# Kernel tuning notes

Hardware: AMD Instinct MI355X
Metric: run time of the kernel (lower is better)

Reference implementation:

```python
import jax, jax.numpy as jnp
import numpy as np

B, T, D_IN, H, K, C = 8, 2048, 512, 384, 8192, 8
N_BLOCKS = 6
EPS = 1e-5


def conv1d(x, w, b, pad, groups=1):
    # x: [B, Cin, T], w: [Cout, Cin//groups, k]
    y = jax.lax.conv_general_dilated(
        x, w, window_strides=(1,), padding=[(pad, pad)],
        dimension_numbers=("NCH", "OIH", "NCH"), feature_group_count=groups)
    return y + b[None, :, None]


def layernorm(x, g, b):
    # normalize over last axis
    m = jnp.mean(x, axis=-1, keepdims=True)
    v = jnp.mean(jnp.square(x - m), axis=-1, keepdims=True)
    return (x - m) * jax.lax.rsqrt(v + EPS) * g + b


def setup_inputs() -> dict:
    key = jax.random.key(0)
    ks = iter(jax.random.split(key, 32))
    s = 0.02
    inp = {
        "x": jax.random.normal(next(ks), (B, T, D_IN), dtype=jnp.float32),
        "enc_w": jax.random.normal(next(ks), (H, D_IN, 7)) * s,
        "enc_b": jnp.zeros((H,)),
        "enc_ln_g": jnp.ones((H,)),
        "enc_ln_b": jnp.zeros((H,)),
        "blk_dw_w": jax.random.normal(next(ks), (N_BLOCKS, H, 1, 7)) * s,
        "blk_dw_b": jnp.zeros((N_BLOCKS, H)),
        "blk_ln_g": jnp.ones((N_BLOCKS, H)),
        "blk_ln_b": jnp.zeros((N_BLOCKS, H)),
        "blk_w1": jax.random.normal(next(ks), (N_BLOCKS, 4 * H, H)) * s,
        "blk_b1": jnp.zeros((N_BLOCKS, 4 * H)),
        "blk_w2": jax.random.normal(next(ks), (N_BLOCKS, H, 4 * H)) * s,
        "blk_b2": jnp.zeros((N_BLOCKS, H)),
        "out_w": jax.random.normal(next(ks), (C, H, 1)) * s,
        "out_b": jnp.zeros((C,)),
        "embeddings": jax.random.normal(next(ks), (K, C)),
    }
    return inp


def encode(x, enc_w, enc_b, enc_ln_g, enc_ln_b, blk_dw_w, blk_dw_b,
           blk_ln_g, blk_ln_b, blk_w1, blk_b1, blk_w2, blk_b2, out_w, out_b):
    h = x.transpose(0, 2, 1)                       # [B, D_IN, T]
    h = conv1d(h, enc_w, enc_b, pad=3)             # [B, H, T]
    h = layernorm(h.transpose(0, 2, 1), enc_ln_g, enc_ln_b).transpose(0, 2, 1)
    for i in range(N_BLOCKS):
        res = h
        h = conv1d(h, blk_dw_w[i], blk_dw_b[i], pad=3, groups=H)  # depthwise
        ht = h.transpose(0, 2, 1)                  # [B, T, H]
        ht = layernorm(ht, blk_ln_g[i], blk_ln_b[i])
        ht = jnp.einsum("bth,fh->btf", ht, blk_w1[i]) + blk_b1[i]
        ht = jax.nn.gelu(ht, approximate=False)    # torch GELU is exact erf
        ht = jnp.einsum("btf,hf->bth", ht, blk_w2[i]) + blk_b2[i]
        h = ht.transpose(0, 2, 1) + res
    z = conv1d(h, out_w, out_b, pad=0)             # [B, C, T]
    return z.transpose(0, 2, 1)                    # [B, T, C]


def reference(x, enc_w, enc_b, enc_ln_g, enc_ln_b, blk_dw_w, blk_dw_b,
              blk_ln_g, blk_ln_b, blk_w1, blk_b1, blk_w2, blk_b2,
              out_w, out_b, embeddings):
    z = encode(x, enc_w, enc_b, enc_ln_g, enc_ln_b, blk_dw_w, blk_dw_b,
               blk_ln_g, blk_ln_b, blk_w1, blk_b1, blk_w2, blk_b2, out_w, out_b)
    flat = z.reshape(-1, C)                        # [B*T, C]
    # squared euclidean distances: same argmin as torch.cdist
    d2 = (jnp.sum(flat * flat, axis=1, keepdims=True)
          - 2.0 * flat @ embeddings.T
          + jnp.sum(embeddings * embeddings, axis=1))  # [B*T, K]
    indices = jnp.argmin(d2, axis=1)               # [B*T], int
    return indices
```

## Files before the change

kernel.cpp:

```cpp
#include <hip/hip_runtime.h>
#include <math.h>

#define T_   2048
#define DIN  512
#define H_   384
#define H4_  1536
#define BT_  16384

typedef _Float16 half_t;
typedef _Float16 f16x8 __attribute__((ext_vector_type(8)));
typedef _Float16 f16x4 __attribute__((ext_vector_type(4)));
typedef float f32x4 __attribute__((ext_vector_type(4)));

#define LO_SCALE 2048.0f
#define LO_INV   4.8828125e-4f

__device__ __forceinline__ void lds_barrier() {
    asm volatile("s_waitcnt lgkmcnt(0)\n\ts_barrier" ::: "memory");
}

__device__ __forceinline__ void gload_lds(const half_t* g, half_t* l) {
    __builtin_amdgcn_global_load_lds(
        (const __attribute__((address_space(1))) unsigned int*)(const void*)g,
        (__attribute__((address_space(3))) unsigned int*)(void*)l, 16, 0, 0);
}

__device__ __forceinline__ void split2(float v, half_t* hi, half_t* lo) {
    half_t h = (half_t)v;
    *hi = h;
    *lo = (half_t)((v - (float)h) * LO_SCALE);
}

__global__ void k_split4(const float* __restrict__ in, half_t* __restrict__ hi,
                         half_t* __restrict__ lo, long n4) {
    long i = (long)blockIdx.x * 256 + threadIdx.x;
    if (i >= n4) return;
    float4 v = ((const float4*)in)[i];
    f16x4 vh, vl;
    float a[4] = {v.x, v.y, v.z, v.w};
#pragma unroll
    for (int j = 0; j < 4; ++j) {
        half_t h = (half_t)a[j];
        vh[j] = h;
        vl[j] = (half_t)((a[j] - (float)h) * LO_SCALE);
    }
    ((f16x4*)hi)[i] = vh;
    ((f16x4*)lo)[i] = vl;
}

__global__ void k_split_encw(const float* __restrict__ in, half_t* __restrict__ hi,
                             half_t* __restrict__ lo) {
    int idx = blockIdx.x * 256 + threadIdx.x;
    if (idx >= H_ * 3584) return;
    int n = idx / 3584;
    int r = idx % 3584;
    int tap = r >> 9, i = r & 511;
    split2(in[n * 3584 + i * 7 + tap], hi + idx, lo + idx);
}

__global__ void k_ln(const float* __restrict__ in, float* __restrict__ out,
                     const float* __restrict__ g, const float* __restrict__ b) {
    int row = blockIdx.x;
    int lane = threadIdx.x;
    const float* ir = in + (long)row * H_;
    float v[6];
    float s = 0.f;
#pragma unroll
    for (int j = 0; j < 6; ++j) { v[j] = ir[lane + (j << 6)]; s += v[j]; }
#pragma unroll
    for (int o = 32; o > 0; o >>= 1) s += __shfl_down(s, o, 64);
    s = __shfl(s, 0, 64);
    float mean = s * (1.f / 384.f);
    float q = 0.f;
#pragma unroll
    for (int j = 0; j < 6; ++j) { float d = v[j] - mean; q += d * d; }
#pragma unroll
    for (int o = 32; o > 0; o >>= 1) q += __shfl_down(q, o, 64);
    q = __shfl(q, 0, 64);
    float rstd = rsqrtf(q * (1.f / 384.f) + 1e-5f);
    float* orow = out + (long)row * H_;
#pragma unroll
    for (int j = 0; j < 6; ++j) {
        int c = lane + (j << 6);
        orow[c] = (v[j] - mean) * rstd * g[c] + b[c];
    }
}

__global__ __launch_bounds__(256) void k_dwconv_ln(
    const float* __restrict__ h, half_t* __restrict__ oh,
    half_t* __restrict__ ol,
    const float* __restrict__ w, const float* __restrict__ wb,
    const float* __restrict__ g, const float* __restrict__ gb) {
    int row = (blockIdx.x << 2) + (threadIdx.x >> 6);
    int b = row >> 11;
    int t = row & 2047;
    int lane = threadIdx.x & 63;
    const float* hb = h + ((long)b * T_) * H_;
    float vx[3], vy[3];
    float s = 0.f;
#pragma unroll
    for (int j = 0; j < 3; ++j) {
        int c = (lane << 1) + (j << 7);
        float ax = wb[c], ay = wb[c + 1];
        const float* wcx = w + c * 7;
        const float* wcy = wcx + 7;
#pragma unroll
        for (int k = 0; k < 7; ++k) {
            int tt = t + k - 3;
            if ((unsigned)tt < (unsigned)T_) {
                float2 hv = *(const float2*)&hb[(long)tt * H_ + c];
                ax = fmaf(hv.x, wcx[k], ax);
                ay = fmaf(hv.y, wcy[k], ay);
            }
        }
        vx[j] = ax; vy[j] = ay;
        s += ax + ay;
    }
#pragma unroll
    for (int o = 32; o > 0; o >>= 1) s += __shfl_down(s, o, 64);
    s = __shfl(s, 0, 64);
    float mean = s * (1.f / 384.f);
    float q = 0.f;
#pragma unroll
    for (int j = 0; j < 3; ++j) {
        float dx = vx[j] - mean, dy = vy[j] - mean;
        q += dx * dx + dy * dy;
    }
#pragma unroll
    for (int o = 32; o > 0; o >>= 1) q += __shfl_down(q, o, 64);
    q = __shfl(q, 0, 64);
    float rstd = rsqrtf(q * (1.f / 384.f) + 1e-5f);
    long ro = (long)row * H_;
#pragma unroll
    for (int j = 0; j < 3; ++j) {
        int c = (lane << 1) + (j << 7);
        float valx = (vx[j] - mean) * rstd * g[c] + gb[c];
        float valy = (vy[j] - mean) * rstd * g[c + 1] + gb[c + 1];
        split2(valx, oh + ro + c, ol + ro + c);
        split2(valy, oh + ro + c + 1, ol + ro + c + 1);
    }
}

#define DECLSET(S) float4 pAh##S, pAl##S, pBh0##S, pBl0##S, pBh1##S, pBl1##S

#define LOADREGS(S, k0_) do {                                               \
    int k0v = (k0_);                                                        \
    if (MODE == 0) {                                                        \
        int kk = k0v + ak;                                                  \
        int tap = kk >> 9, ii = kk & 511;                                   \
        int ta = tt0 + tap;                                                 \
        pAh##S = pAl##S = make_float4(0.f, 0.f, 0.f, 0.f);                  \
        if ((unsigned)ta < 2048u) {                                         \
            long o = ((long)bq * 2048 + ta) * 512 + ii;                     \
            pAh##S = *(const float4*)(Ah + o);                              \
            pAl##S = *(const float4*)(Al + o);                              \
        }                                                                   \
    } else {                                                                \
        pAh##S = *(const float4*)(Ah + aoff + k0v);                         \
        pAl##S = *(const float4*)(Al + aoff + k0v);                         \
    }                                                                       \
    pBh0##S = *(const float4*)(Bh + boff0 + k0v);                           \
    pBl0##S = *(const float4*)(Bl + boff0 + k0v);                           \
    pBh1##S = *(const float4*)(Bh + boff1 + k0v);                           \
    pBl1##S = *(const float4*)(Bl + boff1 + k0v);                           \
} while (0)

#define STOREBUF(S, buf) do {                                               \
    *(float4*)&smem[(buf) * 2048 + aw] = pAh##S;                            \
    *(float4*)&smem[4096 + (buf) * 2048 + aw] = pAl##S;                     \
    int b_ = 8192 + (buf) * 4096 + aw;                                      \
    *(float4*)&smem[b_] = pBh0##S;                                          \
    *(float4*)&smem[b_ + 2048] = pBh1##S;                                   \
    *(float4*)&smem[b_ + 8192] = pBl0##S;                                   \
    *(float4*)&smem[b_ + 8192 + 2048] = pBl1##S;                            \
} while (0)

template <int MODE, int NN>
__global__ __launch_bounds__(256, 3) void k_mgemm64(
    const half_t* __restrict__ Ah, const half_t* __restrict__ Al,
    const half_t* __restrict__ Bh, const half_t* __restrict__ Bl,
    const float* __restrict__ bias, const float* __restrict__ res,
    float* __restrict__ Cf, half_t* __restrict__ Ch, half_t* __restrict__ Cl,
    int N, int K) {
    __shared__ __align__(16) half_t smem[24576];
    const int tid = threadIdx.x;
    const int lane = tid & 63, wid = tid >> 6;
    const int wn = wid << 5;
    const int quad = lane >> 4, l16 = lane & 15;

    constexpr int NWG = 256 * NN;
    constexpr int CHUNK = NWG / 8;
    const int lin = blockIdx.x;
    const int tile = (lin & 7) * CHUNK + (lin >> 3);
    const int m0 = (tile / NN) << 6;
    const int n0 = (tile % NN) << 7;

    const int ar = tid >> 2;
    const int ak = (tid & 3) << 3;

    long aoff = 0;
    int tt0 = 0, bq = 0;
    if (MODE == 0) {
        bq = m0 >> 11;
        tt0 = (m0 & 2047) + ar - 3;
    } else {
        aoff = (long)(m0 + ar) * K + ak;
    }
    const long boff0 = (long)(n0 + ar) * K + ak;
    const long boff1 = boff0 + (long)64 * K;

    const int aw = ar * 32 + ((((tid & 3) ^ (ar >> 1)) & 3) << 3);

    DECLSET(0);
    DECLSET(1);

    f32x4 acc1[4][2] = {};
    f32x4 acc2[4][2] = {};
    const int sw = ((quad ^ (l16 >> 1)) & 3) << 3;

    auto compute = [&](int buf) {
        const int ab = buf * 2048 + l16 * 32 + sw;
        const int bb = 8192 + buf * 4096 + (wn + l16) * 32 + sw;
        f16x8 fah[4], fal[4], fgh[2], fgl[2];
#pragma unroll
        for (int f = 0; f < 4; ++f) {
            fah[f] = *(const f16x8*)&smem[ab + f * 512];
            fal[f] = *(const f16x8*)&smem[ab + 4096 + f * 512];
        }
#pragma unroll
        for (int g = 0; g < 2; ++g) {
            fgh[g] = *(const f16x8*)&smem[bb + g * 512];
            fgl[g] = *(const f16x8*)&smem[bb + 8192 + g * 512];
        }
#pragma unroll
        for (int f = 0; f < 4; ++f)
#pragma unroll
            for (int g = 0; g < 2; ++g)
                acc2[f][g] = __builtin_amdgcn_mfma_f32_16x16x32_f16(fah[f], fgl[g], acc2[f][g], 0, 0, 0);
#pragma unroll
        for (int f = 0; f < 4; ++f)
#pragma unroll
            for (int g = 0; g < 2; ++g)
                acc2[f][g] = __builtin_amdgcn_mfma_f32_16x16x32_f16(fal[f], fgh[g], acc2[f][g], 0, 0, 0);
#pragma unroll
        for (int f = 0; f < 4; ++f)
#pragma unroll
            for (int g = 0; g < 2; ++g)
                acc1[f][g] = __builtin_amdgcn_mfma_f32_16x16x32_f16(fah[f], fgh[g], acc1[f][g], 0, 0, 0);
    };

    const int nIter = K >> 5;
    LOADREGS(0, 0);
    LOADREGS(1, 32);
    STOREBUF(0, 0);
    if (nIter > 2) LOADREGS(0, 64);
    for (int it = 0; it < nIter; it += 2) {
        lds_barrier();
        compute(0);
        STOREBUF(1, 1);
        if (it + 3 < nIter) LOADREGS(1, (it + 3) << 5);
        lds_barrier();
        compute(1);
        if (it + 2 < nIter) {
            STOREBUF(0, 0);
            if (it + 4 < nIter) LOADREGS(0, (it + 4) << 5);
        }
    }

    float bv[2];
    bv[0] = bias[n0 + wn + l16];
    bv[1] = bias[n0 + wn + 16 + l16];

#pragma unroll
    for (int f = 0; f < 4; ++f)
#pragma unroll
        for (int g = 0; g < 2; ++g)
#pragma unroll
            for (int r = 0; r < 4; ++r) {
                long row = m0 + f * 16 + quad * 4 + r;
                int col = n0 + wn + g * 16 + l16;
                float v = acc1[f][g][r] + acc2[f][g][r] * LO_INV + bv[g];
                long o = row * N + col;
                if (MODE == 2) v += res[o];
                Cf[o] = v;
            }
}

template <int MODE, int NT>
__global__ __launch_bounds__(512, 2) void k_g192p(
    const half_t* __restrict__ Ah, const half_t* __restrict__ Al,
    const half_t* __restrict__ Bh, const half_t* __restrict__ Bl,
    const float* __restrict__ bias, const float* __restrict__ res,
    float* __restrict__ Cf, half_t* __restrict__ Ch, half_t* __restrict__ Cl,
    int N, int K) {
    __shared__ __align__(16) half_t smem[61440];
    const int tid = threadIdx.x;
    const int lane = tid & 63, wid = tid >> 6;
    const int wm = (wid & 1) << 6;
    const int wn = ((wid >> 1) & 3) * 48;
    const int quad = lane >> 4, l16 = lane & 15;

    constexpr int NWG = 128 * NT;
    constexpr int CHUNK = NWG / 8;
    const int lin = blockIdx.x;
    const int tile = (lin & 7) * CHUNK + (lin >> 3);
    const int m0 = (tile / NT) << 7;
    const int n0 = (tile % NT) * 192;

    const int lr = lane >> 2;
    const int lg = (lane & 3) ^ ((lane >> 3) & 3);
    const half_t* gsrc[5];
    int ldo[5];
#pragma unroll
    for (int j = 0; j < 5; ++j) {
        int q = wid * 5 + j;
        const half_t* sp;
        long r0;
        int lo_;
        if (q < 8)       { sp = Ah; r0 = m0 + q * 16;        lo_ = q * 512; }
        else if (q < 16) { sp = Al; r0 = m0 + (q - 8) * 16;  lo_ = 4096 + (q - 8) * 512; }
        else if (q < 28) { sp = Bh; r0 = n0 + (q - 16) * 16; lo_ = 8192 + (q - 16) * 512; }
        else             { sp = Bl; r0 = n0 + (q - 28) * 16; lo_ = 14336 + (q - 28) * 512; }
        gsrc[j] = sp + (r0 + lr) * (long)K + lg * 8;
        ldo[j] = lo_;
    }

#define STAGE3(bufb, k0_) do {                                              \
    int k0v = (k0_);                                                        \
    _Pragma("unroll")                                                       \
    for (int j = 0; j < 5; ++j)                                             \
        gload_lds(gsrc[j] + k0v, &smem[(bufb) + ldo[j]]);                   \
} while (0)

    f32x4 acc1[4][3] = {};
    f32x4 acc2[4][3] = {};
    const int sw = ((quad ^ (l16 >> 1)) & 3) << 3;

    const int nIter = K >> 5;
    STAGE3(0, 0);
    STAGE3(20480, 32);
    int b0 = 0, b1 = 20480, b2 = 40960;
    for (int it = 0; it < nIter; ++it) {
        if (it + 1 < nIter)
            asm volatile("s_waitcnt vmcnt(5)" ::: "memory");
        else
            asm volatile("s_waitcnt vmcnt(0)" ::: "memory");
        __builtin_amdgcn_s_barrier();
        __builtin_amdgcn_sched_barrier(0);

        const int ab = b0 + (wm + l16) * 32 + sw;
        const int bb = b0 + 8192 + (wn + l16) * 32 + sw;
        const int k2 = (it + 2) << 5;
        const bool st = (it + 2 < nIter);
        f16x8 fah[4], fal[4], fgh[3], fgl[3];

#pragma unroll
        for (int f = 0; f < 4; ++f)
            fah[f] = *(const f16x8*)&smem[ab + f * 512];
#pragma unroll
        for (int g = 0; g < 3; ++g)
            fgl[g] = *(const f16x8*)&smem[bb + 6144 + g * 512];
        if (st) {
            gload_lds(gsrc[0] + k2, &smem[b2 + ldo[0]]);
            gload_lds(gsrc[1] + k2, &smem[b2 + ldo[1]]);
        }
        __builtin_amdgcn_s_barrier();
        __builtin_amdgcn_sched_barrier(0);
        __builtin_amdgcn_s_setprio(1);
#pragma unroll
        for (int f = 0; f < 4; ++f)
#pragma unroll
            for (int g = 0; g < 3; ++g)
                acc2[f][g] = __builtin_amdgcn_mfma_f32_16x16x32_f16(fah[f], fgl[g], acc2[f][g], 0, 0, 0);
        __builtin_amdgcn_s_setprio(0);
        __builtin_amdgcn_sched_barrier(0);
        __builtin_amdgcn_s_barrier();

#pragma unroll
        for (int f = 0; f < 4; ++f)
            fal[f] = *(const f16x8*)&smem[ab + 4096 + f * 512];
#pragma unroll
        for (int g = 0; g < 3; ++g)
            fgh[g] = *(const f16x8*)&smem[bb + g * 512];
        if (st) {
            gload_lds(gsrc[2] + k2, &smem[b2 + ldo[2]]);
            gload_lds(gsrc[3] + k2, &smem[b2 + ldo[3]]);
            gload_lds(gsrc[4] + k2, &smem[b2 + ldo[4]]);
        }
        __builtin_amdgcn_s_barrier();
        __builtin_amdgcn_sched_barrier(0);
        __builtin_amdgcn_s_setprio(1);
#pragma unroll
        for (int f = 0; f < 4; ++f)
#pragma unroll
            for (int g = 0; g < 3; ++g)
                acc2[f][g] = __builtin_amdgcn_mfma_f32_16x16x32_f16(fal[f], fgh[g], acc2[f][g], 0, 0, 0);
        __builtin_amdgcn_s_setprio(0);
        __builtin_amdgcn_sched_barrier(0);
        __builtin_amdgcn_s_barrier();

        __builtin_amdgcn_s_setprio(1);
#pragma unroll
        for (int f = 0; f < 4; ++f)
#pragma unroll
            for (int g = 0; g < 3; ++g)
                acc1[f][g] = __builtin_amdgcn_mfma_f32_16x16x32_f16(fah[f], fgh[g], acc1[f][g], 0, 0, 0);
        __builtin_amdgcn_s_setprio(0);
        __builtin_amdgcn_sched_barrier(0);

        int t_ = b0; b0 = b1; b1 = b2; b2 = t_;
    }
#undef STAGE3

    float bv[3];
#pragma unroll
    for (int g = 0; g < 3; ++g) bv[g] = bias[n0 + wn + g * 16 + l16];

    if (MODE == 1) {
        __syncthreads();
#pragma unroll
        for (int f = 0; f < 4; ++f)
#pragma unroll
            for (int g = 0; g < 3; ++g)
#pragma unroll
                for (int r = 0; r < 4; ++r) {
                    int rm = wm + f * 16 + quad * 4 + r;
                    int cn = wn + g * 16 + l16;
                    float v = acc1[f][g][r] + acc2[f][g][r] * LO_INV + bv[g];
                    v = 0.5f * v * (1.0f + erff(v * 0.70710678118654752f));
                    half_t hh = (half_t)v;
                    smem[rm * 200 + cn] = hh;
                    smem[25600 + rm * 200 + cn] = (half_t)((v - (float)hh) * LO_SCALE);
                }
        __syncthreads();
        int row = tid >> 2, c0 = (tid & 3) * 48;
        long go = (long)(m0 + row) * N + n0 + c0;
        int so = row * 200 + c0;
#pragma unroll
        for (int u = 0; u < 6; ++u) {
            *(float4*)(Ch + go + u * 8) = *(const float4*)&smem[so + u * 8];
            *(float4*)(Cl + go + u * 8) = *(const float4*)&smem[25600 + so + u * 8];
        }
    } else {
#pragma unroll
        for (int f = 0; f < 4; ++f)
#pragma unroll
            for (int g = 0; g < 3; ++g)
#pragma unroll
                for (int r = 0; r < 4; ++r) {
                    long row = m0 + wm + f * 16 + quad * 4 + r;
                    int col = n0 + wn + g * 16 + l16;
                    float v = acc1[f][g][r] + acc2[f][g][r] * LO_INV + bv[g];
                    long o = row * N + col;
                    v += res[o];
                    Cf[o] = v;
                }
    }
}

__global__ __launch_bounds__(256) void k_outconv_argmin(
    const float* __restrict__ h, const float* __restrict__ ow,
    const float* __restrict__ ob, const float* __restrict__ emb,
    int* __restrict__ outIdx) {
    __shared__ float hs[16][H_ + 1];
    __shared__ float zs[16][8];
    __shared__ float es[16 * 516];
    __shared__ float rb[16][16];
    __shared__ int ri[16][16];
    const int tid = threadIdx.x;
    const int row0 = blockIdx.x << 4;

    for (int i = tid; i < 16 * (H_ / 4); i += 256) {
        int r = i / 96;
        int c4 = (i % 96) << 2;
        float4 v = *(const float4*)&h[((long)(row0 + r)) * H_ + c4];
        hs[r][c4] = v.x; hs[r][c4 + 1] = v.y; hs[r][c4 + 2] = v.z; hs[r][c4 + 3] = v.w;
    }
    __syncthreads();

    if (tid < 128) {
        int r = tid & 15, c = tid >> 4;
        float acc = ob[c];
        const float* wc = ow + c * H_;
        for (int j = 0; j < H_; ++j) acc = fmaf(hs[r][j], wc[j], acc);
        zs[r][c] = acc;
    }
    __syncthreads();

    const int r = tid & 15;
    const int sl = tid >> 4;
    float z0 = zs[r][0], z1 = zs[r][1], z2 = zs[r][2], z3 = zs[r][3];
    float z4 = zs[r][4], z5 = zs[r][5], z6 = zs[r][6], z7 = zs[r][7];
    float best = 3.4e38f;
    int bi = 0;

    for (int ch = 0; ch < 8; ++ch) {
        __syncthreads();
        for (int i = tid; i < 2048; i += 256) {
            int e = i >> 1;
            int half = (i & 1) << 2;
            float4 src = *(const float4*)&emb[(((long)(ch << 10)) + e) * 8 + half];
            *(float4*)&es[(e >> 6) * 516 + ((e & 63) << 3) + half] = src;
        }
        __syncthreads();
        const float* ep = es + sl * 516;
        int gbase = (ch << 10) + (sl << 6);
#pragma unroll 4
        for (int j = 0; j < 64; ++j) {
            float4 e0 = *(const float4*)(ep + (j << 3));
            float4 e1 = *(const float4*)(ep + (j << 3) + 4);
            float t, d;
            t = e0.x - z0; d = t * t;
            t = e0.y - z1; d = fmaf(t, t, d);
            t = e0.z - z2; d = fmaf(t, t, d);
            t = e0.w - z3; d = fmaf(t, t, d);
            t = e1.x - z4; d = fmaf(t, t, d);
            t = e1.y - z5; d = fmaf(t, t, d);
            t = e1.z - z6; d = fmaf(t, t, d);
            t = e1.w - z7; d = fmaf(t, t, d);
            if (d < best) { best = d; bi = gbase + j; }
        }
    }
    rb[r][sl] = best;
    ri[r][sl] = bi;
    __syncthreads();
    if (sl == 0) {
        float bb = rb[r][0];
        int bbi = ri[r][0];
#pragma unroll
        for (int s2 = 1; s2 < 16; ++s2) {
            float v = rb[r][s2];
            int i2 = ri[r][s2];
            if (v < bb || (v == bb && i2 < bbi)) { bb = v; bbi = i2; }
        }
        outIdx[row0 + r] = bbi;
    }
}

extern "C" void kernel_launch(void* const* d_in, const int* in_sizes, int n_in,
                              void* d_out, int out_size, void* d_ws, size_t ws_size,
                              hipStream_t stream) {
    const float* x        = (const float*)d_in[0];
    const float* enc_w    = (const float*)d_in[1];
    const float* enc_b    = (const float*)d_in[2];
    const float* enc_ln_g = (const float*)d_in[3];
    const float* enc_ln_b = (const float*)d_in[4];
    const float* blk_dw_w = (const float*)d_in[5];
    const float* blk_dw_b = (const float*)d_in[6];
    const float* blk_ln_g = (const float*)d_in[7];
    const float* blk_ln_b = (const float*)d_in[8];
    const float* blk_w1   = (const float*)d_in[9];
    const float* blk_b1   = (const float*)d_in[10];
    const float* blk_w2   = (const float*)d_in[11];
    const float* blk_b2   = (const float*)d_in[12];
    const float* out_w    = (const float*)d_in[13];
    const float* out_b    = (const float*)d_in[14];
    const float* emb      = (const float*)d_in[15];
    int* out = (int*)d_out;

    char* base = (char*)d_ws;
    float*  h    = (float*)base;
    half_t* tmph = (half_t*)(base + 25165824);
    half_t* tmpl = (half_t*)(base + 37748736);
    half_t* ht4h = (half_t*)(base + 50331648);
    half_t* ht4l = (half_t*)(base + 100663296);
    half_t* ench = (half_t*)(base + 150994944);
    half_t* encl = (half_t*)(base + 153747456);
    half_t* w1h  = (half_t*)(base + 156499968);
    half_t* w1l  = (half_t*)(base + 163577856);
    half_t* w2h  = (half_t*)(base + 170655744);
    half_t* w2l  = (half_t*)(base + 177733632);
    half_t* xh = ht4h;
    half_t* xl = (half_t*)(base + 50331648 + 16777216);

    k_split4<<<8192, 256, 0, stream>>>(x, xh, xl, 2097152L);
    k_split4<<<3456, 256, 0, stream>>>(blk_w1, w1h, w1l, 884736L);
    k_split4<<<3456, 256, 0, stream>>>(blk_w2, w2h, w2l, 884736L);
    k_split_encw<<<(H_ * 3584 + 255) / 256, 256, 0, stream>>>(enc_w, ench, encl);

    k_mgemm64<0, 3><<<768, 256, 0, stream>>>(xh, xl, ench, encl, enc_b,
                                             nullptr, h, nullptr, nullptr,
                                             H_, 3584);
    k_ln<<<BT_, 64, 0, stream>>>(h, h, enc_ln_g, enc_ln_b);

    for (int i = 0; i < 6; ++i) {
        k_dwconv_ln<<<BT_ / 4, 256, 0, stream>>>(h, tmph, tmpl, blk_dw_w + i * H_ * 7,
                                                 blk_dw_b + i * H_, blk_ln_g + i * H_,
                                                 blk_ln_b + i * H_);
        k_g192p<1, 8><<<1024, 512, 0, stream>>>(
            tmph, tmpl, w1h + (long)i * 589824, w1l + (long)i * 589824,
            blk_b1 + i * H4_, nullptr, nullptr, ht4h, ht4l, H4_, H_);
        k_g192p<2, 2><<<256, 512, 0, stream>>>(
            ht4h, ht4l, w2h + (long)i * 589824, w2l + (long)i * 589824,
            blk_b2 + i * H_, h, h, nullptr, nullptr, H_, H4_);
    }

    k_outconv_argmin<<<BT_ / 16, 256, 0, stream>>>(h, out_w, out_b, emb, out);
}
```

Before: 1.642 ms.

## Pad input along time and run encoder conv on the pipelined 192-wide GEMM

The input is split into hi/lo fp16 planes written into a time-padded buffer with three zero rows on each side of every batch. Because the seven conv taps then become contiguous strided rows, the encoder im2col GEMM can use the k_g192p kernel's direct global-to-LDS triple-buffered pipeline in place of the older register-staged 64-row kernel. This drops the per-load bounds checks and runs the encoder on the larger tile. In exchange the split kernel writes a slightly larger buffer, and the overlapping-row addressing (row stride 512 with K=3584) relies on the padded layout being exact.

```diff
diff --git a/kernel.cpp b/kernel.cpp
--- a/kernel.cpp
+++ b/kernel.cpp
@@ -14,10 +14,6 @@
 
 #define LO_SCALE 2048.0f
 #define LO_INV   4.8828125e-4f
-
-__device__ __forceinline__ void lds_barrier() {
-    asm volatile("s_waitcnt lgkmcnt(0)\n\ts_barrier" ::: "memory");
-}
 
 __device__ __forceinline__ void gload_lds(const half_t* g, half_t* l) {
     __builtin_amdgcn_global_load_lds(
@@ -43,6 +39,29 @@
         half_t h = (half_t)a[j];
         vh[j] = h;
         vl[j] = (half_t)((a[j] - (float)h) * LO_SCALE);
+    }
+    ((f16x4*)hi)[i] = vh;
+    ((f16x4*)lo)[i] = vl;
+}
+
+__global__ void k_split_pad(const float* __restrict__ in, half_t* __restrict__ hi,
+                            half_t* __restrict__ lo) {
+    long i = (long)blockIdx.x * 256 + threadIdx.x;
+    if (i >= 2103296L) return;
+    int ii4 = (int)(i & 127);
+    long rest = i >> 7;
+    int u = (int)(rest % 2054);
+    int b = (int)(rest / 2054);
+    f16x4 vh = (f16x4)(half_t)0.f, vl = (f16x4)(half_t)0.f;
+    if (u >= 3 && u < 2051) {
+        float4 v = ((const float4*)in)[((long)b * 2048 + (u - 3)) * 128 + ii4];
+        float a[4] = {v.x, v.y, v.z, v.w};
+#pragma unroll
+        for (int j = 0; j < 4; ++j) {
+            half_t h = (half_t)a[j];
+            vh[j] = h;
+            vl[j] = (half_t)((a[j] - (float)h) * LO_SCALE);
+        }
     }
     ((f16x4*)hi)[i] = vh;
     ((f16x4*)lo)[i] = vl;
@@ -139,151 +158,6 @@
         split2(valx, oh + ro + c, ol + ro + c);
         split2(valy, oh + ro + c + 1, ol + ro + c + 1);
     }
-}
-
-#define DECLSET(S) float4 pAh##S, pAl##S, pBh0##S, pBl0##S, pBh1##S, pBl1##S
-
-#define LOADREGS(S, k0_) do {                                               \
-    int k0v = (k0_);                                                        \
-    if (MODE == 0) {                                                        \
-        int kk = k0v + ak;                                                  \
-        int tap = kk >> 9, ii = kk & 511;                                   \
-        int ta = tt0 + tap;                                                 \
-        pAh##S = pAl##S = make_float4(0.f, 0.f, 0.f, 0.f);                  \
-        if ((unsigned)ta < 2048u) {                                         \
-            long o = ((long)bq * 2048 + ta) * 512 + ii;                     \
-            pAh##S = *(const float4*)(Ah + o);                              \
-            pAl##S = *(const float4*)(Al + o);                              \
-        }                                                                   \
-    } else {                                                                \
-        pAh##S = *(const float4*)(Ah + aoff + k0v);                         \
-        pAl##S = *(const float4*)(Al + aoff + k0v);                         \
-    }                                                                       \
-    pBh0##S = *(const float4*)(Bh + boff0 + k0v);                           \
-    pBl0##S = *(const float4*)(Bl + boff0 + k0v);                           \
-    pBh1##S = *(const float4*)(Bh + boff1 + k0v);                           \
-    pBl1##S = *(const float4*)(Bl + boff1 + k0v);                           \
-} while (0)
-
-#define STOREBUF(S, buf) do {                                               \
-    *(float4*)&smem[(buf) * 2048 + aw] = pAh##S;                            \
-    *(float4*)&smem[4096 + (buf) * 2048 + aw] = pAl##S;                     \
-    int b_ = 8192 + (buf) * 4096 + aw;                                      \
-    *(float4*)&smem[b_] = pBh0##S;                                          \
-    *(float4*)&smem[b_ + 2048] = pBh1##S;                                   \
-    *(float4*)&smem[b_ + 8192] = pBl0##S;                                   \
-    *(float4*)&smem[b_ + 8192 + 2048] = pBl1##S;                            \
-} while (0)
-
-template <int MODE, int NN>
-__global__ __launch_bounds__(256, 3) void k_mgemm64(
-    const half_t* __restrict__ Ah, const half_t* __restrict__ Al,
-    const half_t* __restrict__ Bh, const half_t* __restrict__ Bl,
-    const float* __restrict__ bias, const float* __restrict__ res,
-    float* __restrict__ Cf, half_t* __restrict__ Ch, half_t* __restrict__ Cl,
-    int N, int K) {
-    __shared__ __align__(16) half_t smem[24576];
-    const int tid = threadIdx.x;
-    const int lane = tid & 63, wid = tid >> 6;
-    const int wn = wid << 5;
-    const int quad = lane >> 4, l16 = lane & 15;
-
-    constexpr int NWG = 256 * NN;
-    constexpr int CHUNK = NWG / 8;
-    const int lin = blockIdx.x;
-    const int tile = (lin & 7) * CHUNK + (lin >> 3);
-    const int m0 = (tile / NN) << 6;
-    const int n0 = (tile % NN) << 7;
-
-    const int ar = tid >> 2;
-    const int ak = (tid & 3) << 3;
-
-    long aoff = 0;
-    int tt0 = 0, bq = 0;
-    if (MODE == 0) {
-        bq = m0 >> 11;
-        tt0 = (m0 & 2047) + ar - 3;
-    } else {
-        aoff = (long)(m0 + ar) * K + ak;
-    }
-    const long boff0 = (long)(n0 + ar) * K + ak;
-    const long boff1 = boff0 + (long)64 * K;
-
-    const int aw = ar * 32 + ((((tid & 3) ^ (ar >> 1)) & 3) << 3);
-
-    DECLSET(0);
-    DECLSET(1);
-
-    f32x4 acc1[4][2] = {};
-    f32x4 acc2[4][2] = {};
-    const int sw = ((quad ^ (l16 >> 1)) & 3) << 3;
-
-    auto compute = [&](int buf) {
-        const int ab = buf * 2048 + l16 * 32 + sw;
-        const int bb = 8192 + buf * 4096 + (wn + l16) * 32 + sw;
-        f16x8 fah[4], fal[4], fgh[2], fgl[2];
-#pragma unroll
-        for (int f = 0; f < 4; ++f) {
-            fah[f] = *(const f16x8*)&smem[ab + f * 512];
-            fal[f] = *(const f16x8*)&smem[ab + 4096 + f * 512];
-        }
-#pragma unroll
-        for (int g = 0; g < 2; ++g) {
-            fgh[g] = *(const f16x8*)&smem[bb + g * 512];
-            fgl[g] = *(const f16x8*)&smem[bb + 8192 + g * 512];
-        }
-#pragma unroll
-        for (int f = 0; f < 4; ++f)
-#pragma unroll
-            for (int g = 0; g < 2; ++g)
-                acc2[f][g] = __builtin_amdgcn_mfma_f32_16x16x32_f16(fah[f], fgl[g], acc2[f][g], 0, 0, 0);
-#pragma unroll
-        for (int f = 0; f < 4; ++f)
-#pragma unroll
-            for (int g = 0; g < 2; ++g)
-                acc2[f][g] = __builtin_amdgcn_mfma_f32_16x16x32_f16(fal[f], fgh[g], acc2[f][g], 0, 0, 0);
-#pragma unroll
-        for (int f = 0; f < 4; ++f)
-#pragma unroll
-            for (int g = 0; g < 2; ++g)
-                acc1[f][g] = __builtin_amdgcn_mfma_f32_16x16x32_f16(fah[f], fgh[g], acc1[f][g], 0, 0, 0);
-    };
-
-    const int nIter = K >> 5;
-    LOADREGS(0, 0);
-    LOADREGS(1, 32);
-    STOREBUF(0, 0);
-    if (nIter > 2) LOADREGS(0, 64);
-    for (int it = 0; it < nIter; it += 2) {
-        lds_barrier();
-        compute(0);
-        STOREBUF(1, 1);
-        if (it + 3 < nIter) LOADREGS(1, (it + 3) << 5);
-        lds_barrier();
-        compute(1);
-        if (it + 2 < nIter) {
-            STOREBUF(0, 0);
-            if (it + 4 < nIter) LOADREGS(0, (it + 4) << 5);
-        }
-    }
-
-    float bv[2];
-    bv[0] = bias[n0 + wn + l16];
-    bv[1] = bias[n0 + wn + 16 + l16];
-
-#pragma unroll
-    for (int f = 0; f < 4; ++f)
-#pragma unroll
-        for (int g = 0; g < 2; ++g)
-#pragma unroll
-            for (int r = 0; r < 4; ++r) {
-                long row = m0 + f * 16 + quad * 4 + r;
-                int col = n0 + wn + g * 16 + l16;
-                float v = acc1[f][g][r] + acc2[f][g][r] * LO_INV + bv[g];
-                long o = row * N + col;
-                if (MODE == 2) v += res[o];
-                Cf[o] = v;
-            }
 }
 
 template <int MODE, int NT>
@@ -307,6 +181,16 @@
     const int m0 = (tile / NT) << 7;
     const int n0 = (tile % NT) * 192;
 
+    long abase;
+    int astr;
+    if (MODE == 0) {
+        abase = (long)(m0 >> 11) * 2054 + (m0 & 2047);
+        astr = 512;
+    } else {
+        abase = m0;
+        astr = K;
+    }
+
     const int lr = lane >> 2;
     const int lg = (lane & 3) ^ ((lane >> 3) & 3);
     const half_t* gsrc[5];
@@ -314,15 +198,19 @@
 #pragma unroll
     for (int j = 0; j < 5; ++j) {
         int q = wid * 5 + j;
-        const half_t* sp;
-        long r0;
-        int lo_;
-        if (q < 8)       { sp = Ah; r0 = m0 + q * 16;        lo_ = q * 512; }
-        else if (q < 16) { sp = Al; r0 = m0 + (q - 8) * 16;  lo_ = 4096 + (q - 8) * 512; }
-        else if (q < 28) { sp = Bh; r0 = n0 + (q - 16) * 16; lo_ = 8192 + (q - 16) * 512; }
-        else             { sp = Bl; r0 = n0 + (q - 28) * 16; lo_ = 14336 + (q - 28) * 512; }
-        gsrc[j] = sp + (r0 + lr) * (long)K + lg * 8;
-        ldo[j] = lo_;
+        if (q < 8) {
+            gsrc[j] = Ah + (abase + q * 16 + lr) * (long)astr + lg * 8;
+            ldo[j] = q * 512;
+        } else if (q < 16) {
+            gsrc[j] = Al + (abase + (q - 8) * 16 + lr) * (long)astr + lg * 8;
+            ldo[j] = 4096 + (q - 8) * 512;
+        } else if (q < 28) {
+            gsrc[j] = Bh + ((long)(n0 + (q - 16) * 16 + lr)) * K + lg * 8;
+            ldo[j] = 8192 + (q - 16) * 512;
+        } else {
+            gsrc[j] = Bl + ((long)(n0 + (q - 28) * 16 + lr)) * K + lg * 8;
+            ldo[j] = 14336 + (q - 28) * 512;
+        }
     }
 
 #define STAGE3(bufb, k0_) do {                                              \
@@ -452,7 +340,7 @@
                     int col = n0 + wn + g * 16 + l16;
                     float v = acc1[f][g][r] + acc2[f][g][r] * LO_INV + bv[g];
                     long o = row * N + col;
-                    v += res[o];
+                    if (MODE == 2) v += res[o];
                     Cf[o] = v;
                 }
     }
@@ -570,17 +458,17 @@
     half_t* w1l  = (half_t*)(base + 163577856);
     half_t* w2h  = (half_t*)(base + 170655744);
     half_t* w2l  = (half_t*)(base + 177733632);
-    half_t* xh = ht4h;
-    half_t* xl = (half_t*)(base + 50331648 + 16777216);
-
-    k_split4<<<8192, 256, 0, stream>>>(x, xh, xl, 2097152L);
+    half_t* xph = (half_t*)(base + 50331648);
+    half_t* xpl = (half_t*)(base + 50331648 + 16826368);
+
+    k_split_pad<<<8216, 256, 0, stream>>>(x, xph, xpl);
     k_split4<<<3456, 256, 0, stream>>>(blk_w1, w1h, w1l, 884736L);
     k_split4<<<3456, 256, 0, stream>>>(blk_w2, w2h, w2l, 884736L);
     k_split_encw<<<(H_ * 3584 + 255) / 256, 256, 0, stream>>>(enc_w, ench, encl);
 
-    k_mgemm64<0, 3><<<768, 256, 0, stream>>>(xh, xl, ench, encl, enc_b,
-                                             nullptr, h, nullptr, nullptr,
-                                             H_, 3584);
+    k_g192p<0, 2><<<256, 512, 0, stream>>>(xph, xpl, ench, encl, enc_b,
+                                           nullptr, h, nullptr, nullptr,
+                                           H_, 3584);
     k_ln<<<BT_, 64, 0, stream>>>(h, h, enc_ln_g, enc_ln_b);
 
     for (int i = 0; i < 6; ++i) {
```

After: 1.702 ms. 1.04x slower.
